# Kernel optimization log

Measured on AMD Instinct MI355X. Metric: run time of the kernel, lower is better.

## Reference

```python
import jax, jax.numpy as jnp
import numpy as np

HIDDEN = 64
HALF = 32
VOCAB = 64
B, L = 256, 2048


def _l2norm(x):
    # matches torch F.normalize(dim=-1, eps=1e-12)
    return x / jnp.maximum(jnp.linalg.norm(x, axis=-1, keepdims=True), 1e-12)


def setup_inputs() -> dict:
    key = jax.random.key(0)
    ks = jax.random.split(key, 16)
    s = 0.02
    return {
        "seq": jax.random.randint(ks[0], (B, L), 0, VOCAB),
        "embed": jax.random.normal(ks[1], (VOCAB, HIDDEN), jnp.float32) * s,
        "W1": jax.random.normal(ks[2], (2 * HIDDEN, HIDDEN), jnp.float32) * s,
        "b1": jnp.zeros((2 * HIDDEN,), jnp.float32),
        "W2": jax.random.normal(ks[3], (HIDDEN, 2 * HIDDEN), jnp.float32) * s,
        "b2": jnp.zeros((HIDDEN,), jnp.float32),
        "ln_g": jnp.ones((HIDDEN,), jnp.float32),
        "ln_b": jnp.zeros((HIDDEN,), jnp.float32),
        "Ws": jax.random.normal(ks[4], (HALF, HIDDEN), jnp.float32) * s,
        "bs": jnp.zeros((HALF,), jnp.float32),
        "We": jax.random.normal(ks[5], (HALF, HIDDEN), jnp.float32) * s,
        "be": jnp.zeros((HALF,), jnp.float32),
        "Wrp": jax.random.normal(ks[6], (HIDDEN, 2 * HALF), jnp.float32) * s,
        "brp": jnp.zeros((HIDDEN,), jnp.float32),
        "Wo": jax.random.normal(ks[7], (VOCAB, HIDDEN), jnp.float32) * s,
        "bo": jnp.zeros((VOCAB,), jnp.float32),
    }


def reference(seq, embed, W1, b1, W2, b2, ln_g, ln_b, Ws, bs, We, be, Wrp, brp, Wo, bo):
    # Encoder: embed -> LayerNorm(h + FF(h))
    h0 = embed[seq]                                     # [B,L,H]
    ff = jnp.maximum(h0 @ W1.T + b1, 0.0) @ W2.T + b2
    x = h0 + ff
    mu = x.mean(-1, keepdims=True)
    var = x.var(-1, keepdims=True)
    h = (x - mu) / jnp.sqrt(var + 1e-5) * ln_g + ln_b   # [B,L,H]

    Bn, Ln, _ = h.shape
    half = Ws.shape[0]
    hs_all = h @ Ws.T + bs                              # [B,L,half]
    he_all = h @ We.T + be

    # sequential delta-rule memory writes over t = 0 .. L-2
    hs_seq = jnp.swapaxes(hs_all[:, :-1], 0, 1)         # [L-1,B,half]
    he_seq = jnp.swapaxes(he_all[:, :-1], 0, 1)
    scales = (jnp.arange(1, Ln) / Ln).astype(h.dtype)   # (t+1)/L
    M0 = jnp.zeros((Bn, half, half), h.dtype)

    def step(carry, inp):
        M_s, M_e = carry
        hs, he, sc = inp
        ks_ = _l2norm(hs)
        ke_ = _l2norm(he)
        vps = jnp.einsum('bij,bj->bi', M_s, ks_)
        vpe = jnp.einsum('bij,bj->bi', M_e, ke_)
        M_s = M_s + (hs - vps)[:, :, None] * ks_[:, None, :]
        M_e = M_e + sc * (he - vpe)[:, :, None] * ke_[:, None, :]
        return (M_s, M_e), None

    (M_s, M_e), _ = jax.lax.scan(step, (M0, M0), (hs_seq, he_seq, scales))

    # read with last-position query
    qs = _l2norm(hs_all[:, -1])
    qe = _l2norm(he_all[:, -1])
    rs = jnp.einsum('bij,bj->bi', M_s, qs)
    re = jnp.einsum('bij,bj->bi', M_e, qe)
    r = jnp.concatenate([rs, re], axis=-1)              # [B, 2*half]
    return (r @ Wrp.T + brp) @ Wo.T + bo                # [B, vocab]
```

## Files before the change

kernel.cpp:

```cpp
#include <hip/hip_runtime.h>

#define HIDDEN 64
#define HALFD  32
#define VOCAB  64
#define BATCH  256
#define SEQLEN 2048

#define RLF(v, sl) __int_as_float(__builtin_amdgcn_readlane(__float_as_int(v), (sl)))
#define RLI(v, sl) __builtin_amdgcn_readlane((v), (sl))
#define SWZF(v, j) __int_as_float(__builtin_amdgcn_ds_swizzle(__float_as_int(v), ((j) << 5)))
#define SWZE(v)    __int_as_float(__builtin_amdgcn_ds_swizzle(__float_as_int(v), 0x0007))
#define GIX(j,m) (((j)==0?0:(j)==1?7:(j)==2?13:(j)==3?18:(j)==4?22:(j)==5?25:27) + (m) - (j) - 1)
#define OM(m) (((m)*((m)+1))>>1)

__global__ __launch_bounds__(256) void vocab_kernel(
    const float* __restrict__ embed, const float* __restrict__ W1, const float* __restrict__ b1,
    const float* __restrict__ W2, const float* __restrict__ b2,
    const float* __restrict__ ln_g, const float* __restrict__ ln_b,
    const float* __restrict__ Ws, const float* __restrict__ bs,
    const float* __restrict__ We, const float* __restrict__ be,
    float* __restrict__ ws)
{
    const int v = blockIdx.x;
    const int tid = threadIdx.x;

    __shared__ float e_s[64];
    __shared__ float W1_s[128][65];
    __shared__ float W2_s[64][129];
    __shared__ float Wse_s[64][65];
    __shared__ float a1_s[128];
    __shared__ float h_s[64];

    if (tid < 64) e_s[tid] = embed[v * 64 + tid];
    {
        const float4* src = (const float4*)W1;
        for (int i = tid; i < 2048; i += 256) {
            float4 x4 = src[i];
            const int e = i << 2, r = e >> 6, c = e & 63;
            W1_s[r][c] = x4.x; W1_s[r][c+1] = x4.y; W1_s[r][c+2] = x4.z; W1_s[r][c+3] = x4.w;
        }
    }
    __syncthreads();

    if (tid < 128) {
        float p0 = b1[tid], p1 = 0.f, p2 = 0.f, p3 = 0.f;
        #pragma unroll
        for (int m = 0; m < 64; m += 4) {
            p0 = fmaf(e_s[m],   W1_s[tid][m],   p0);
            p1 = fmaf(e_s[m+1], W1_s[tid][m+1], p1);
            p2 = fmaf(e_s[m+2], W1_s[tid][m+2], p2);
            p3 = fmaf(e_s[m+3], W1_s[tid][m+3], p3);
        }
        a1_s[tid] = fmaxf((p0 + p1) + (p2 + p3), 0.0f);
    } else {
        const float4* src = (const float4*)W2;
        for (int i = tid - 128; i < 2048; i += 128) {
            float4 x4 = src[i];
            const int e = i << 2, r = e >> 7, c = e & 127;
            W2_s[r][c] = x4.x; W2_s[r][c+1] = x4.y; W2_s[r][c+2] = x4.z; W2_s[r][c+3] = x4.w;
        }
    }
    __syncthreads();

    if (tid < 64) {
        float f0 = b2[tid], f1 = 0.f, f2 = 0.f, f3 = 0.f;
        #pragma unroll
        for (int m = 0; m < 128; m += 4) {
            f0 = fmaf(a1_s[m],   W2_s[tid][m],   f0);
            f1 = fmaf(a1_s[m+1], W2_s[tid][m+1], f1);
            f2 = fmaf(a1_s[m+2], W2_s[tid][m+2], f2);
            f3 = fmaf(a1_s[m+3], W2_s[tid][m+3], f3);
        }
        float x = e_s[tid] + ((f0 + f1) + (f2 + f3));
        float s = x, s2 = x * x;
        #pragma unroll
        for (int off = 32; off >= 1; off >>= 1) {
            s  += __shfl_xor(s,  off, 64);
            s2 += __shfl_xor(s2, off, 64);
        }
        float mu  = s * (1.0f / 64.0f);
        float var = s2 * (1.0f / 64.0f) - mu * mu;
        h_s[tid] = (x - mu) * rsqrtf(var + 1e-5f) * ln_g[tid] + ln_b[tid];
    } else if (tid < 192) {
        const int t2 = tid - 64;
        const float4* s1 = (const float4*)Ws;
        const float4* s2 = (const float4*)We;
        for (int i = t2; i < 512; i += 128) {
            float4 x4 = s1[i];
            const int e = i << 2, r = e >> 6, c = e & 63;
            Wse_s[r][c] = x4.x; Wse_s[r][c+1] = x4.y; Wse_s[r][c+2] = x4.z; Wse_s[r][c+3] = x4.w;
        }
        for (int i = t2; i < 512; i += 128) {
            float4 x4 = s2[i];
            const int e = i << 2, r = e >> 6, c = e & 63;
            Wse_s[32+r][c] = x4.x; Wse_s[32+r][c+1] = x4.y; Wse_s[32+r][c+2] = x4.z; Wse_s[32+r][c+3] = x4.w;
        }
    }
    __syncthreads();

    if (tid < 64) {
        const int j = tid & 31;
        const bool is_s = tid < 32;
        float c0 = is_s ? bs[j] : be[j];
        float c1 = 0.f, c2 = 0.f, c3 = 0.f;
        #pragma unroll
        for (int m = 0; m < 64; m += 4) {
            c0 = fmaf(h_s[m],   Wse_s[tid][m],   c0);
            c1 = fmaf(h_s[m+1], Wse_s[tid][m+1], c1);
            c2 = fmaf(h_s[m+2], Wse_s[tid][m+2], c2);
            c3 = fmaf(h_s[m+3], Wse_s[tid][m+3], c3);
        }
        float acc = (c0 + c1) + (c2 + c3);

        float n2 = acc * acc;
        #pragma unroll
        for (int off = 16; off >= 1; off >>= 1) n2 += __shfl_xor(n2, off, 64);
        float norm = sqrtf(n2);
        float kn = acc / fmaxf(norm, 1e-12f);

        const int base = v * 32 + j;
        if (is_s) { ws[base]        = kn; ws[4096 + base] = acc; }
        else      { ws[2048 + base] = kn; ws[6144 + base] = acc; }
    }
}

__global__ __launch_bounds__(256) void gram_kernel(float* __restrict__ ws)
{
    const int w   = blockIdx.x & 1;
    const int seg = blockIdx.x >> 1;
    const int tid = threadIdx.x;
    __shared__ float k_s[64][33];
    const float* kb = ws + w * 2048;
    for (int i = tid; i < 2048; i += 256) k_s[i >> 5][i & 31] = kb[i];
    __syncthreads();
    const int a  = seg * 16 + (tid >> 4);
    const int b0 = (tid & 15) << 2;
    float* Gw = ws + 8192 + w * 4096 + a * 64;
    #pragma unroll
    for (int bb = 0; bb < 4; ++bb) {
        const int bcol = b0 + bb;
        float acc0 = 0.f, acc1 = 0.f;
        #pragma unroll
        for (int m = 0; m < 32; m += 2) {
            acc0 = fmaf(k_s[a][m],     k_s[bcol][m],     acc0);
            acc1 = fmaf(k_s[a][m + 1], k_s[bcol][m + 1], acc1);
        }
        Gw[bcol] = acc0 + acc1;
    }
}

static __device__ __forceinline__ void build_wpack(
    const int* tj, float fb, float invL, bool is_e, bool is_last, float* Wp,
    const float* __restrict__ Gg)
{
    float f[8];
    #pragma unroll
    for (int j = 0; j < 8; ++j) f[j] = is_e ? (fb + (float)j * invL) : 1.0f;
    if (is_last) f[7] = 0.0f;

    float g[28];
    #pragma unroll
    for (int j = 0; j < 7; ++j)
        #pragma unroll
        for (int m = j + 1; m < 8; ++m) g[GIX(j, m)] = Gg[tj[j] * 64 + tj[m]];

    #pragma unroll
    for (int m = 0; m < 8; ++m) {
        float col[8];
        col[m] = f[m];
        #pragma unroll
        for (int j = 6; j >= 0; --j) {
            if (j < m) {
                float acc = 0.0f;
                #pragma unroll
                for (int p = 1; p < 8; ++p)
                    if (p > j && p <= m) acc = fmaf(g[GIX(j, p)], col[p], acc);
                col[j] = -f[j] * acc;
            }
        }
        #pragma unroll
        for (int j = 0; j < 8; ++j)
            if (j <= m) Wp[OM(m) + j] = col[j];
    }
}

struct C16 {
    int   tokv;
    int   tk[16];
    float grow[16];
    float R1[8];
    float R2[8];
    float braw;
    float bpp[16];
    float gx[8];
};

__global__ __launch_bounds__(128) void scan_kernel(
    const int* __restrict__ seq, const float* __restrict__ ws,
    const float* __restrict__ Wrp, const float* __restrict__ brp,
    const float* __restrict__ Wo, const float* __restrict__ bo,
    float* __restrict__ out)
{
    const int b    = blockIdx.x;
    const int tid  = threadIdx.x;
    const int w    = tid >> 6;
    const int lane = tid & 63;
    const int l7   = lane & 7;
    const int l15  = lane & 15;
    const bool is_e = (w == 1);

    __shared__ __align__(16) float Wlds[2][256][8][8];
    __shared__ __align__(16) int   toklds[SEQLEN];
    __shared__ float wacc_s[2][64];
    __shared__ float r_s[64];
    __shared__ float t1_s[64];

    const float* Gg = ws + 8192 + w * 4096;
    const int*   sq = seq + b * SEQLEN;

    {
        const int4* sq4 = (const int4*)sq;
        int4* tl4 = (int4*)toklds;
        #pragma unroll
        for (int i = 0; i < 4; ++i) tl4[tid + i * 128] = sq4[tid + i * 128];
    }
    __syncthreads();

    {
        const float invL = 1.0f / (float)SEQLEN;
        #pragma unroll
        for (int qq = 0; qq < 4; ++qq) {
            const int c = lane + (qq << 6);
            int tj[8];
            #pragma unroll
            for (int j = 0; j < 8; ++j) tj[j] = toklds[c * 8 + j];
            float Wp[36];
            build_wpack(tj, (float)(8 * c + 1) * invL, invL, is_e, c == 255, Wp, Gg);
            const int cx = c & 7;
            #pragma unroll
            for (int i = 0; i < 8; ++i) {
                float r[8];
                #pragma unroll
                for (int m = 0; m < 8; ++m) r[m] = (m >= i) ? Wp[OM(m) + i] : 0.0f;
                float4* dst = (float4*)&Wlds[w][c][i ^ cx][0];
                dst[0] = make_float4(r[0], r[1], r[2], r[3]);
                dst[1] = make_float4(r[4], r[5], r[6], r[7]);
            }
        }
    }
    __syncthreads();

    C16 A, B;
    float u, wc0 = 0.f, wc1 = 0.f, wc2 = 0.f, wc3 = 0.f;
    float sp[16];
    int tv2;

    A.tokv = sq[127 * 16 + l15];
    B.tokv = sq[126 * 16 + l15];
    tv2    = sq[125 * 16 + l15];
    #pragma unroll
    for (int j = 0; j < 16; ++j) A.tk[j] = RLI(A.tokv, j);
    #pragma unroll
    for (int j = 0; j < 16; ++j) A.grow[j] = Gg[A.tk[j] * 64 + lane];
    {
        const float4* rp = (const float4*)&Wlds[w][255][l7 ^ 7][0];
        float4 lo = rp[0], hi = rp[1];
        A.R1[0]=lo.x; A.R1[1]=lo.y; A.R1[2]=lo.z; A.R1[3]=lo.w;
        A.R1[4]=hi.x; A.R1[5]=hi.y; A.R1[6]=hi.z; A.R1[7]=hi.w;
        const float4* rq = (const float4*)&Wlds[w][254][l7 ^ 6][0];
        float4 lo2 = rq[0], hi2 = rq[1];
        A.R2[0]=lo2.x; A.R2[1]=lo2.y; A.R2[2]=lo2.z; A.R2[3]=lo2.w;
        A.R2[4]=hi2.x; A.R2[5]=hi2.y; A.R2[6]=hi2.z; A.R2[7]=hi2.w;
    }
    u = Gg[A.tk[15] * 64 + lane];
    A.braw = __shfl(u, A.tokv, 64);
    B.braw = __shfl(u, B.tokv, 64);
    #pragma unroll
    for (int j = 0; j < 16; ++j) A.bpp[j] = 0.0f;
    {
        int addrE = __shfl(A.tokv, l7, 64);
        #pragma unroll
        for (int j = 0; j < 8; ++j) A.gx[j] = Gg[A.tk[8 + j] * 64 + addrE];
    }
    #pragma unroll
    for (int j = 0; j < 16; ++j) sp[j] = 0.0f;

    auto body16 = [&](C16& cur, C16& nxt, int C) {
        const int cm1 = (C > 0) ? C - 1 : 0;
        const int cm3 = (C > 2) ? C - 3 : 0;

        float q0 = fmaf(cur.bpp[1],  sp[1],  cur.bpp[0]  * sp[0]);
        float q1 = fmaf(cur.bpp[3],  sp[3],  cur.bpp[2]  * sp[2]);
        float q2 = fmaf(cur.bpp[5],  sp[5],  cur.bpp[4]  * sp[4]);
        float q3 = fmaf(cur.bpp[7],  sp[7],  cur.bpp[6]  * sp[6]);
        float q4 = fmaf(cur.bpp[9],  sp[9],  cur.bpp[8]  * sp[8]);
        float q5 = fmaf(cur.bpp[11], sp[11], cur.bpp[10] * sp[10]);
        float q6 = fmaf(cur.bpp[13], sp[13], cur.bpp[12] * sp[12]);
        float q7 = fmaf(cur.bpp[15], sp[15], cur.bpp[14] * sp[14]);
        float tl = cur.braw - (((q0 + q1) + (q2 + q3)) + ((q4 + q5) + (q6 + q7)));

        float tL0 = SWZF(tl, 8),  tL1 = SWZF(tl, 9),  tL2 = SWZF(tl, 10), tL3 = SWZF(tl, 11);
        float tL4 = SWZF(tl, 12), tL5 = SWZF(tl, 13), tL6 = SWZF(tl, 14), tL7 = SWZF(tl, 15);
        float tE  = SWZE(tl);

        #pragma unroll
        for (int j = 0; j < 16; ++j) nxt.bpp[j] = __shfl(cur.grow[j], nxt.tokv, 64);
        #pragma unroll
        for (int j = 0; j < 16; ++j) nxt.tk[j] = RLI(nxt.tokv, j);
        #pragma unroll
        for (int j = 0; j < 16; ++j) nxt.grow[j] = Gg[nxt.tk[j] * 64 + lane];
        {
            const int c8a = 2 * cm1 + 1, c8b = 2 * cm1;
            const float4* rp = (const float4*)&Wlds[w][c8a][l7 ^ (c8a & 7)][0];
            float4 lo = rp[0], hi = rp[1];
            nxt.R1[0]=lo.x; nxt.R1[1]=lo.y; nxt.R1[2]=lo.z; nxt.R1[3]=lo.w;
            nxt.R1[4]=hi.x; nxt.R1[5]=hi.y; nxt.R1[6]=hi.z; nxt.R1[7]=hi.w;
            const float4* rq = (const float4*)&Wlds[w][c8b][l7 ^ (c8b & 7)][0];
            float4 lo2 = rq[0], hi2 = rq[1];
            nxt.R2[0]=lo2.x; nxt.R2[1]=lo2.y; nxt.R2[2]=lo2.z; nxt.R2[3]=lo2.w;
            nxt.R2[4]=hi2.x; nxt.R2[5]=hi2.y; nxt.R2[6]=hi2.z; nxt.R2[7]=hi2.w;
        }
        {
            int addrE = __shfl(nxt.tokv, l7, 64);
            #pragma unroll
            for (int j = 0; j < 8; ++j) nxt.gx[j] = Gg[nxt.tk[8 + j] * 64 + addrE];
        }
        int tv3 = sq[cm3 * 16 + l15];

        const float* R1 = cur.R1;
        float a0 = fmaf(R1[1], tL1, R1[0] * tL0);
        float a1 = fmaf(R1[3], tL3, R1[2] * tL2);
        float a2 = fmaf(R1[5], tL5, R1[4] * tL4);
        float a3 = fmaf(R1[7], tL7, R1[6] * tL6);
        float sd1 = (a0 + a1) + (a2 + a3);
        float s10 = SWZF(sd1, 0), s11 = SWZF(sd1, 1), s12 = SWZF(sd1, 2), s13 = SWZF(sd1, 3);
        float s14 = SWZF(sd1, 4), s15 = SWZF(sd1, 5), s16 = SWZF(sd1, 6), s17 = SWZF(sd1, 7);

        const float* gx = cur.gx;
        float b0 = fmaf(gx[1], s11, gx[0] * s10);
        float b1 = fmaf(gx[3], s13, gx[2] * s12);
        float b2 = fmaf(gx[5], s15, gx[4] * s14);
        float b3 = fmaf(gx[7], s17, gx[6] * s16);
        float tpl = tE - ((b0 + b1) + (b2 + b3));
        float tP0 = SWZF(tpl, 0), tP1 = SWZF(tpl, 1), tP2 = SWZF(tpl, 2), tP3 = SWZF(tpl, 3);
        float tP4 = SWZF(tpl, 4), tP5 = SWZF(tpl, 5), tP6 = SWZF(tpl, 6), tP7 = SWZF(tpl, 7);

        const float* R2 = cur.R2;
        float e0 = fmaf(R2[1], tP1, R2[0] * tP0);
        float e1 = fmaf(R2[3], tP3, R2[2] * tP2);
        float e2 = fmaf(R2[5], tP5, R2[4] * tP4);
        float e3 = fmaf(R2[7], tP7, R2[6] * tP6);
        float sd2 = (e0 + e1) + (e2 + e3);
        float s20 = SWZF(sd2, 0), s21 = SWZF(sd2, 1), s22 = SWZF(sd2, 2), s23 = SWZF(sd2, 3);
        float s24 = SWZF(sd2, 4), s25 = SWZF(sd2, 5), s26 = SWZF(sd2, 6), s27 = SWZF(sd2, 7);

        float dA = fmaf(cur.grow[8],  s10, fmaf(cur.grow[9],  s11, fmaf(cur.grow[10], s12, cur.grow[11] * s13)));
        float dB = fmaf(cur.grow[12], s14, fmaf(cur.grow[13], s15, fmaf(cur.grow[14], s16, cur.grow[15] * s17)));
        float dC = fmaf(cur.grow[0],  s20, fmaf(cur.grow[1],  s21, fmaf(cur.grow[2],  s22, cur.grow[3]  * s23)));
        float dD = fmaf(cur.grow[4],  s24, fmaf(cur.grow[5],  s25, fmaf(cur.grow[6],  s26, cur.grow[7]  * s27)));
        u -= (dA + dB) + (dC + dD);
        cur.braw = __shfl(u, tv2, 64);

        wc0 += (lane == cur.tk[8])  ? s10 : 0.0f;
        wc1 += (lane == cur.tk[9])  ? s11 : 0.0f;
        wc2 += (lane == cur.tk[10]) ? s12 : 0.0f;
        wc3 += (lane == cur.tk[11]) ? s13 : 0.0f;
        wc0 += (lane == cur.tk[12]) ? s14 : 0.0f;
        wc1 += (lane == cur.tk[13]) ? s15 : 0.0f;
        wc2 += (lane == cur.tk[14]) ? s16 : 0.0f;
        wc3 += (lane == cur.tk[15]) ? s17 : 0.0f;
        wc0 += (lane == cur.tk[0])  ? s20 : 0.0f;
        wc1 += (lane == cur.tk[1])  ? s21 : 0.0f;
        wc2 += (lane == cur.tk[2])  ? s22 : 0.0f;
        wc3 += (lane == cur.tk[3])  ? s23 : 0.0f;
        wc0 += (lane == cur.tk[4])  ? s24 : 0.0f;
        wc1 += (lane == cur.tk[5])  ? s25 : 0.0f;
        wc2 += (lane == cur.tk[6])  ? s26 : 0.0f;
        wc3 += (lane == cur.tk[7])  ? s27 : 0.0f;

        cur.tokv = tv2; tv2 = tv3;
        sp[8]  = s10; sp[9]  = s11; sp[10] = s12; sp[11] = s13;
        sp[12] = s14; sp[13] = s15; sp[14] = s16; sp[15] = s17;
        sp[0]  = s20; sp[1]  = s21; sp[2]  = s22; sp[3]  = s23;
        sp[4]  = s24; sp[5]  = s25; sp[6]  = s26; sp[7]  = s27;
    };

    for (int C = 127; C >= 1; C -= 2) {
        body16(A, B, C);
        body16(B, A, C - 1);
    }

    wacc_s[w][lane] = (wc0 + wc1) + (wc2 + wc3);
    __syncthreads();

    if (tid < 64) {
        const int w2  = tid >> 5;
        const int rho = tid & 31;
        const float* vv = ws + 4096 + w2 * 2048;
        const float* wa = &wacc_s[w2][0];
        float acc = 0.0f;
        #pragma unroll 8
        for (int tok = 0; tok < 64; ++tok) acc = fmaf(wa[tok], vv[tok * 32 + rho], acc);
        r_s[tid] = acc;
    }
    __syncthreads();

    if (tid < 64) {
        float acc = brp[tid];
        #pragma unroll 8
        for (int m = 0; m < 64; ++m) acc = fmaf(Wrp[tid * 64 + m], r_s[m], acc);
        t1_s[tid] = acc;
    }
    __syncthreads();
    if (tid < 64) {
        float acc = bo[tid];
        #pragma unroll 8
        for (int m = 0; m < 64; ++m) acc = fmaf(Wo[tid * 64 + m], t1_s[m], acc);
        out[b * 64 + tid] = acc;
    }
}

extern "C" void kernel_launch(void* const* d_in, const int* in_sizes, int n_in,
                              void* d_out, int out_size, void* d_ws, size_t ws_size,
                              hipStream_t stream)
{
    const int*   seq   = (const int*)  d_in[0];
    const float* embed = (const float*)d_in[1];
    const float* W1    = (const float*)d_in[2];
    const float* b1    = (const float*)d_in[3];
    const float* W2    = (const float*)d_in[4];
    const float* b2    = (const float*)d_in[5];
    const float* ln_g  = (const float*)d_in[6];
    const float* ln_b  = (const float*)d_in[7];
    const float* Ws    = (const float*)d_in[8];
    const float* bs    = (const float*)d_in[9];
    const float* We    = (const float*)d_in[10];
    const float* be    = (const float*)d_in[11];
    const float* Wrp   = (const float*)d_in[12];
    const float* brp   = (const float*)d_in[13];
    const float* Wo    = (const float*)d_in[14];
    const float* bo    = (const float*)d_in[15];
    float* ws  = (float*)d_ws;
    float* out = (float*)d_out;

    hipLaunchKernelGGL(vocab_kernel, dim3(VOCAB), dim3(256), 0, stream,
                       embed, W1, b1, W2, b2, ln_g, ln_b, Ws, bs, We, be, ws);
    hipLaunchKernelGGL(gram_kernel, dim3(8), dim3(256), 0, stream, ws);
    hipLaunchKernelGGL(scan_kernel, dim3(BATCH), dim3(128), 0, stream,
                       seq, ws, Wrp, brp, Wo, bo, out);
}
```

Measured before the change: 207.1 us.

## Precompute fused 16x16 chunk solve matrix to shorten serial dependency chain

Instead of solving each 16-token chunk as two chained 8x8 triangular solves with a cross-coupling Gram term in the serial loop, the prologue now precomputes a combined 16x16 block matrix per chunk (both triangular factors plus the off-diagonal product -W1*Gx*W2) and stores it in packed form in LDS. The serial loop then does one 16-wide matvec with one round of swizzles per chunk, removing a swizzle/FMA/swizzle stage and the per-step gx gathers from the critical path. The cost is a heavier prologue (extra 8x8x8 products per chunk) and irregular per-lane LDS offsets with a zero pad slot for the row loads.

```diff
diff --git a/kernel.cpp b/kernel.cpp
--- a/kernel.cpp
+++ b/kernel.cpp
@@ -6,11 +6,8 @@
 #define BATCH  256
 #define SEQLEN 2048
 
-#define RLF(v, sl) __int_as_float(__builtin_amdgcn_readlane(__float_as_int(v), (sl)))
 #define RLI(v, sl) __builtin_amdgcn_readlane((v), (sl))
 #define SWZF(v, j) __int_as_float(__builtin_amdgcn_ds_swizzle(__float_as_int(v), ((j) << 5)))
-#define SWZE(v)    __int_as_float(__builtin_amdgcn_ds_swizzle(__float_as_int(v), 0x0007))
-#define GIX(j,m) (((j)==0?0:(j)==1?7:(j)==2?13:(j)==3?18:(j)==4?22:(j)==5?25:27) + (m) - (j) - 1)
 #define OM(m) (((m)*((m)+1))>>1)
 
 __global__ __launch_bounds__(256) void vocab_kernel(
@@ -162,7 +159,8 @@
     #pragma unroll
     for (int j = 0; j < 7; ++j)
         #pragma unroll
-        for (int m = j + 1; m < 8; ++m) g[GIX(j, m)] = Gg[tj[j] * 64 + tj[m]];
+        for (int m = j + 1; m < 8; ++m)
+            g[OM(m - 1) + j] = Gg[tj[j] * 64 + tj[m]];
 
     #pragma unroll
     for (int m = 0; m < 8; ++m) {
@@ -174,7 +172,7 @@
                 float acc = 0.0f;
                 #pragma unroll
                 for (int p = 1; p < 8; ++p)
-                    if (p > j && p <= m) acc = fmaf(g[GIX(j, p)], col[p], acc);
+                    if (p > j && p <= m) acc = fmaf(g[OM(p - 1) + j], col[p], acc);
                 col[j] = -f[j] * acc;
             }
         }
@@ -188,11 +186,9 @@
     int   tokv;
     int   tk[16];
     float grow[16];
-    float R1[8];
-    float R2[8];
+    float row[16];
     float braw;
     float bpp[16];
-    float gx[8];
 };
 
 __global__ __launch_bounds__(128) void scan_kernel(
@@ -205,11 +201,10 @@
     const int tid  = threadIdx.x;
     const int w    = tid >> 6;
     const int lane = tid & 63;
-    const int l7   = lane & 7;
     const int l15  = lane & 15;
     const bool is_e = (w == 1);
 
-    __shared__ __align__(16) float Wlds[2][256][8][8];
+    __shared__ __align__(16) float Wlds[2][128][137];
     __shared__ __align__(16) int   toklds[SEQLEN];
     __shared__ float wacc_s[2][64];
     __shared__ float r_s[64];
@@ -226,26 +221,75 @@
     }
     __syncthreads();
 
+    int offR[16];
+    {
+        const bool early = (l15 < 8);
+        const int  ie    = early ? l15 : (l15 - 8);
+        const int  rst   = 8 * ie - (ie * (ie - 1)) / 2;
+        #pragma unroll
+        for (int m = 0; m < 8; ++m)
+            offR[m] = (early && m >= ie) ? (rst + m - ie) : 136;
+        #pragma unroll
+        for (int n = 0; n < 8; ++n)
+            offR[8 + n] = early ? (72 + 8 * ie + n)
+                                : ((n >= ie) ? (36 + rst + n - ie) : 136);
+    }
+
     {
         const float invL = 1.0f / (float)SEQLEN;
         #pragma unroll
-        for (int qq = 0; qq < 4; ++qq) {
-            const int c = lane + (qq << 6);
-            int tj[8];
-            #pragma unroll
-            for (int j = 0; j < 8; ++j) tj[j] = toklds[c * 8 + j];
-            float Wp[36];
-            build_wpack(tj, (float)(8 * c + 1) * invL, invL, is_e, c == 255, Wp, Gg);
-            const int cx = c & 7;
+        for (int qq = 0; qq < 2; ++qq) {
+            const int C = lane + (qq << 6);
+            int tE[8], tL[8];
+            #pragma unroll
+            for (int m = 0; m < 8; ++m) tE[m] = toklds[C * 16 + m];
+            #pragma unroll
+            for (int q = 0; q < 8; ++q) tL[q] = toklds[C * 16 + 8 + q];
+            float Wp2[36], Wp1[36];
+            build_wpack(tE, (float)(16 * C + 1) * invL, invL, is_e, false,    Wp2, Gg);
+            build_wpack(tL, (float)(16 * C + 9) * invL, invL, is_e, C == 127, Wp1, Gg);
+
+            float* WL = &Wlds[w][C][0];
+            int ptr = 0;
+            #pragma unroll
+            for (int i = 0; i < 8; ++i)
+                #pragma unroll
+                for (int m = 0; m < 8; ++m)
+                    if (m >= i) WL[ptr++] = Wp2[OM(m) + i];
+            #pragma unroll
+            for (int q = 0; q < 8; ++q)
+                #pragma unroll
+                for (int n = 0; n < 8; ++n)
+                    if (n >= q) WL[ptr++] = Wp1[OM(n) + q];
+
+            float Gx[64];
+            #pragma unroll
+            for (int q = 0; q < 8; ++q)
+                #pragma unroll
+                for (int m = 0; m < 8; ++m)
+                    Gx[q * 8 + m] = Gg[tL[q] * 64 + tE[m]];
+
             #pragma unroll
             for (int i = 0; i < 8; ++i) {
-                float r[8];
-                #pragma unroll
-                for (int m = 0; m < 8; ++m) r[m] = (m >= i) ? Wp[OM(m) + i] : 0.0f;
-                float4* dst = (float4*)&Wlds[w][c][i ^ cx][0];
-                dst[0] = make_float4(r[0], r[1], r[2], r[3]);
-                dst[1] = make_float4(r[4], r[5], r[6], r[7]);
+                float p[8];
+                #pragma unroll
+                for (int q = 0; q < 8; ++q) {
+                    float acc = 0.0f;
+                    #pragma unroll
+                    for (int m = 0; m < 8; ++m)
+                        if (m >= i) acc = fmaf(Wp2[OM(m) + i], Gx[q * 8 + m], acc);
+                    p[q] = acc;
+                }
+                #pragma unroll
+                for (int n = 0; n < 8; ++n) {
+                    float acc = 0.0f;
+                    #pragma unroll
+                    for (int q = 0; q < 8; ++q)
+                        if (q <= n) acc = fmaf(p[q], Wp1[OM(n) + q], acc);
+                    WL[72 + 8 * i + n] = -acc;
+                }
             }
+            WL[136] = 0.0f;
         }
     }
     __syncthreads();
@@ -263,25 +307,15 @@
     #pragma unroll
     for (int j = 0; j < 16; ++j) A.grow[j] = Gg[A.tk[j] * 64 + lane];
     {
-        const float4* rp = (const float4*)&Wlds[w][255][l7 ^ 7][0];
-        float4 lo = rp[0], hi = rp[1];
-        A.R1[0]=lo.x; A.R1[1]=lo.y; A.R1[2]=lo.z; A.R1[3]=lo.w;
-        A.R1[4]=hi.x; A.R1[5]=hi.y; A.R1[6]=hi.z; A.R1[7]=hi.w;
-        const float4* rq = (const float4*)&Wlds[w][254][l7 ^ 6][0];
-        float4 lo2 = rq[0], hi2 = rq[1];
-        A.R2[0]=lo2.x; A.R2[1]=lo2.y; A.R2[2]=lo2.z; A.R2[3]=lo2.w;
-        A.R2[4]=hi2.x; A.R2[5]=hi2.y; A.R2[6]=hi2.z; A.R2[7]=hi2.w;
+        const float* WL = &Wlds[w][127][0];
+        #pragma unroll
+        for (int m = 0; m < 16; ++m) A.row[m] = WL[offR[m]];
     }
     u = Gg[A.tk[15] * 64 + lane];
     A.braw = __shfl(u, A.tokv, 64);
     B.braw = __shfl(u, B.tokv, 64);
     #pragma unroll
     for (int j = 0; j < 16; ++j) A.bpp[j] = 0.0f;
-    {
-        int addrE = __shfl(A.tokv, l7, 64);
-        #pragma unroll
-        for (int j = 0; j < 8; ++j) A.gx[j] = Gg[A.tk[8 + j] * 64 + addrE];
-    }
     #pragma unroll
     for (int j = 0; j < 16; ++j) sp[j] = 0.0f;
 
@@ -299,9 +333,10 @@
         float q7 = fmaf(cur.bpp[15], sp[15], cur.bpp[14] * sp[14]);
         float tl = cur.braw - (((q0 + q1) + (q2 + q3)) + ((q4 + q5) + (q6 + q7)));
 
-        float tL0 = SWZF(tl, 8),  tL1 = SWZF(tl, 9),  tL2 = SWZF(tl, 10), tL3 = SWZF(tl, 11);
-        float tL4 = SWZF(tl, 12), tL5 = SWZF(tl, 13), tL6 = SWZF(tl, 14), tL7 = SWZF(tl, 15);
-        float tE  = SWZE(tl);
+        float t0 = SWZF(tl, 0),  t1 = SWZF(tl, 1),  t2 = SWZF(tl, 2),  t3 = SWZF(tl, 3);
+        float t4 = SWZF(tl, 4),  t5 = SWZF(tl, 5),  t6 = SWZF(tl, 6),  t7 = SWZF(tl, 7);
+        float t8 = SWZF(tl, 8),  t9 = SWZF(tl, 9),  tA = SWZF(tl, 10), tB = SWZF(tl, 11);
+        float tC = SWZF(tl, 12), tD = SWZF(tl, 13), tE = SWZF(tl, 14), tF = SWZF(tl, 15);
 
         #pragma unroll
         for (int j = 0; j < 16; ++j) nxt.bpp[j] = __shfl(cur.grow[j], nxt.tokv, 64);
@@ -309,80 +344,59 @@
         for (int j = 0; j < 16; ++j) nxt.tk[j] = RLI(nxt.tokv, j);
         #pragma unroll
         for (int j = 0; j < 16; ++j) nxt.grow[j] = Gg[nxt.tk[j] * 64 + lane];
+        int tv3 = sq[cm3 * 16 + l15];
+
+        const float* R = cur.row;
+        float a0 = fmaf(R[1],  t1, R[0]  * t0);
+        float a1 = fmaf(R[3],  t3, R[2]  * t2);
+        float a2 = fmaf(R[5],  t5, R[4]  * t4);
+        float a3 = fmaf(R[7],  t7, R[6]  * t6);
+        float a4 = fmaf(R[9],  t9, R[8]  * t8);
+        float a5 = fmaf(R[11], tB, R[10] * tA);
+        float a6 = fmaf(R[13], tD, R[12] * tC);
+        float a7 = fmaf(R[15], tF, R[14] * tE);
+        float sd = (((a0 + a1) + (a2 + a3)) + ((a4 + a5) + (a6 + a7)));
+
+        float s0 = SWZF(sd, 0),  s1 = SWZF(sd, 1),  s2 = SWZF(sd, 2),  s3 = SWZF(sd, 3);
+        float s4 = SWZF(sd, 4),  s5 = SWZF(sd, 5),  s6 = SWZF(sd, 6),  s7 = SWZF(sd, 7);
+        float s8 = SWZF(sd, 8),  s9 = SWZF(sd, 9),  sA = SWZF(sd, 10), sB = SWZF(sd, 11);
+        float sC = SWZF(sd, 12), sD = SWZF(sd, 13), sE = SWZF(sd, 14), sF = SWZF(sd, 15);
+
         {
-            const int c8a = 2 * cm1 + 1, c8b = 2 * cm1;
-            const float4* rp = (const float4*)&Wlds[w][c8a][l7 ^ (c8a & 7)][0];
-            float4 lo = rp[0], hi = rp[1];
-            nxt.R1[0]=lo.x; nxt.R1[1]=lo.y; nxt.R1[2]=lo.z; nxt.R1[3]=lo.w;
-            nxt.R1[4]=hi.x; nxt.R1[5]=hi.y; nxt.R1[6]=hi.z; nxt.R1[7]=hi.w;
-            const float4* rq = (const float4*)&Wlds[w][c8b][l7 ^ (c8b & 7)][0];
-            float4 lo2 = rq[0], hi2 = rq[1];
-            nxt.R2[0]=lo2.x; nxt.R2[1]=lo2.y; nxt.R2[2]=lo2.z; nxt.R2[3]=lo2.w;
-            nxt.R2[4]=hi2.x; nxt.R2[5]=hi2.y; nxt.R2[6]=hi2.z; nxt.R2[7]=hi2.w;
-        }
-        {
-            int addrE = __shfl(nxt.tokv, l7, 64);
-            #pragma unroll
-            for (int j = 0; j < 8; ++j) nxt.gx[j] = Gg[nxt.tk[8 + j] * 64 + addrE];
-        }
-        int tv3 = sq[cm3 * 16 + l15];
-
-        const float* R1 = cur.R1;
-        float a0 = fmaf(R1[1], tL1, R1[0] * tL0);
-        float a1 = fmaf(R1[3], tL3, R1[2] * tL2);
-        float a2 = fmaf(R1[5], tL5, R1[4] * tL4);
-        float a3 = fmaf(R1[7], tL7, R1[6] * tL6);
-        float sd1 = (a0 + a1) + (a2 + a3);
-        float s10 = SWZF(sd1, 0), s11 = SWZF(sd1, 1), s12 = SWZF(sd1, 2), s13 = SWZF(sd1, 3);
-        float s14 = SWZF(sd1, 4), s15 = SWZF(sd1, 5), s16 = SWZF(sd1, 6), s17 = SWZF(sd1, 7);
-
-        const float* gx = cur.gx;
-        float b0 = fmaf(gx[1], s11, gx[0] * s10);
-        float b1 = fmaf(gx[3], s13, gx[2] * s12);
-        float b2 = fmaf(gx[5], s15, gx[4] * s14);
-        float b3 = fmaf(gx[7], s17, gx[6] * s16);
-        float tpl = tE - ((b0 + b1) + (b2 + b3));
-        float tP0 = SWZF(tpl, 0), tP1 = SWZF(tpl, 1), tP2 = SWZF(tpl, 2), tP3 = SWZF(tpl, 3);
-        float tP4 = SWZF(tpl, 4), tP5 = SWZF(tpl, 5), tP6 = SWZF(tpl, 6), tP7 = SWZF(tpl, 7);
-
-        const float* R2 = cur.R2;
-        float e0 = fmaf(R2[1], tP1, R2[0] * tP0);
-        float e1 = fmaf(R2[3], tP3, R2[2] * tP2);
-        float e2 = fmaf(R2[5], tP5, R2[4] * tP4);
-        float e3 = fmaf(R2[7], tP7, R2[6] * tP6);
-        float sd2 = (e0 + e1) + (e2 + e3);
-        float s20 = SWZF(sd2, 0), s21 = SWZF(sd2, 1), s22 = SWZF(sd2, 2), s23 = SWZF(sd2, 3);
-        float s24 = SWZF(sd2, 4), s25 = SWZF(sd2, 5), s26 = SWZF(sd2, 6), s27 = SWZF(sd2, 7);
-
-        float dA = fmaf(cur.grow[8],  s10, fmaf(cur.grow[9],  s11, fmaf(cur.grow[10], s12, cur.grow[11] * s13)));
-        float dB = fmaf(cur.grow[12], s14, fmaf(cur.grow[13], s15, fmaf(cur.grow[14], s16, cur.grow[15] * s17)));
-        float dC = fmaf(cur.grow[0],  s20, fmaf(cur.grow[1],  s21, fmaf(cur.grow[2],  s22, cur.grow[3]  * s23)));
-        float dD = fmaf(cur.grow[4],  s24, fmaf(cur.grow[5],  s25, fmaf(cur.grow[6],  s26, cur.grow[7]  * s27)));
+            const float* WLn = &Wlds[w][cm1][0];
+            #pragma unroll
+            for (int m = 0; m < 16; ++m) nxt.row[m] = WLn[offR[m]];
+        }
+
+        float dA = fmaf(cur.grow[0],  s0, fmaf(cur.grow[1],  s1, fmaf(cur.grow[2],  s2, cur.grow[3]  * s3)));
+        float dB = fmaf(cur.grow[4],  s4, fmaf(cur.grow[5],  s5, fmaf(cur.grow[6],  s6, cur.grow[7]  * s7)));
+        float dC = fmaf(cur.grow[8],  s8, fmaf(cur.grow[9],  s9, fmaf(cur.grow[10], sA, cur.grow[11] * sB)));
+        float dD = fmaf(cur.grow[12], sC, fmaf(cur.grow[13], sD, fmaf(cur.grow[14], sE, cur.grow[15] * sF)));
         u -= (dA + dB) + (dC + dD);
         cur.braw = __shfl(u, tv2, 64);
 
-        wc0 += (lane == cur.tk[8])  ? s10 : 0.0f;
-        wc1 += (lane == cur.tk[9])  ? s11 : 0.0f;
-        wc2 += (lane == cur.tk[10]) ? s12 : 0.0f;
-        wc3 += (lane == cur.tk[11]) ? s13 : 0.0f;
-        wc0 += (lane == cur.tk[12]) ? s14 : 0.0f;
-        wc1 += (lane == cur.tk[13]) ? s15 : 0.0f;
-        wc2 += (lane == cur.tk[14]) ? s16 : 0.0f;
-        wc3 += (lane == cur.tk[15]) ? s17 : 0.0f;
-        wc0 += (lane == cur.tk[0])  ? s20 : 0.0f;
-        wc1 += (lane == cur.tk[1])  ? s21 : 0.0f;
-        wc2 += (lane == cur.tk[2])  ? s22 : 0.0f;
-        wc3 += (lane == cur.tk[3])  ? s23 : 0.0f;
-        wc0 += (lane == cur.tk[4])  ? s24 : 0.0f;
-        wc1 += (lane == cur.tk[5])  ? s25 : 0.0f;
-        wc2 += (lane == cur.tk[6])  ? s26 : 0.0f;
-        wc3 += (lane == cur.tk[7])  ? s27 : 0.0f;
+        wc0 += (lane == cur.tk[0])  ? s0 : 0.0f;
+        wc1 += (lane == cur.tk[1])  ? s1 : 0.0f;
+        wc2 += (lane == cur.tk[2])  ? s2 : 0.0f;
+        wc3 += (lane == cur.tk[3])  ? s3 : 0.0f;
+        wc0 += (lane == cur.tk[4])  ? s4 : 0.0f;
+        wc1 += (lane == cur.tk[5])  ? s5 : 0.0f;
+        wc2 += (lane == cur.tk[6])  ? s6 : 0.0f;
+        wc3 += (lane == cur.tk[7])  ? s7 : 0.0f;
+        wc0 += (lane == cur.tk[8])  ? s8 : 0.0f;
+        wc1 += (lane == cur.tk[9])  ? s9 : 0.0f;
+        wc2 += (lane == cur.tk[10]) ? sA : 0.0f;
+        wc3 += (lane == cur.tk[11]) ? sB : 0.0f;
+        wc0 += (lane == cur.tk[12]) ? sC : 0.0f;
+        wc1 += (lane == cur.tk[13]) ? sD : 0.0f;
+        wc2 += (lane == cur.tk[14]) ? sE : 0.0f;
+        wc3 += (lane == cur.tk[15]) ? sF : 0.0f;
 
         cur.tokv = tv2; tv2 = tv3;
-        sp[8]  = s10; sp[9]  = s11; sp[10] = s12; sp[11] = s13;
-        sp[12] = s14; sp[13] = s15; sp[14] = s16; sp[15] = s17;
-        sp[0]  = s20; sp[1]  = s21; sp[2]  = s22; sp[3]  = s23;
-        sp[4]  = s24; sp[5]  = s25; sp[6]  = s26; sp[7]  = s27;
+        sp[0] = s0; sp[1] = s1; sp[2]  = s2; sp[3]  = s3;
+        sp[4] = s4; sp[5] = s5; sp[6]  = s6; sp[7]  = s7;
+        sp[8] = s8; sp[9] = s9; sp[10] = sA; sp[11] = sB;
+        sp[12] = sC; sp[13] = sD; sp[14] = sE; sp[15] = sF;
     };
 
     for (int C = 127; C >= 1; C -= 2) {
```

After: 192.0 us. -7.3%, faster.
